# Kernel tuning notes

Measured on AMD Instinct MI355X. Metric: run time of the kernel, lower is better.

The kernel has to match this reference:

```python
import jax, jax.numpy as jnp
import numpy as np

B, C, H, G, NCLS = 32, 256, 128, 128, 2  # graphs, nodes-per-graph==in_channels, hidden, matrix pool, classes
N = B * C                                # total nodes = 8192
E = 131072


def setup_inputs() -> dict:
    key = jax.random.key(0)
    ks = jax.random.split(key, 12)
    gain = 5.0 / 3.0
    xav = gain * np.sqrt(6.0 / (C + C))  # xavier_uniform bound for [C,C]
    return {
        "x": jax.random.normal(ks[0], (N, C), jnp.float32),
        "edge_index": jax.random.randint(ks[1], (2, E), 0, N),
        "graph_id": jax.random.randint(ks[2], (B,), 0, G),
        "batch": jnp.arange(N) // C,
        "pert_W": jax.random.uniform(ks[3], (G, C, C), jnp.float32, -xav, xav),
        "pert_b": jax.random.uniform(ks[4], (G, C, C), jnp.float32, -xav, xav),
        "mask_W": jax.random.uniform(ks[5], (G, C, C), jnp.float32, -xav, xav),
        "gcn_w0": jax.random.normal(ks[6], (C, H), jnp.float32) / np.sqrt(C),
        "gcn_w1": jax.random.normal(ks[7], (H, H), jnp.float32) / np.sqrt(H),
        "gcn_w2": jax.random.normal(ks[8], (H, H), jnp.float32) / np.sqrt(H),
        "mlp_W": jax.random.normal(ks[9], (2 * H, NCLS), jnp.float32) / np.sqrt(2 * H),
        "mlp_b": jnp.zeros((NCLS,), jnp.float32),
    }


def _hard_where(s):
    # MyWhere: 0 if s <= 0.5 else 1
    return jnp.where(s <= 0.5, 0.0, 1.0).astype(s.dtype)


def _predictor(x, adj, batch, gcn_w0, gcn_w1, gcn_w2, mlp_W, mlp_b):
    # GCN encoder: h <- relu(A @ h @ W); readout = concat(mean-pool, max-pool); MLP+sigmoid
    h = x
    for W in (gcn_w0, gcn_w1, gcn_w2):
        h = jax.nn.relu(adj @ (h @ W))
    sums = jax.ops.segment_sum(h, batch, num_segments=B)
    cnt = jax.ops.segment_sum(jnp.ones((h.shape[0], 1), h.dtype), batch, num_segments=B)
    mean = sums / jnp.maximum(cnt, 1.0)
    mx = jax.ops.segment_max(h, batch, num_segments=B)
    pooled = jnp.concatenate([mean, mx], axis=-1)  # [B, 2H]
    return jax.nn.sigmoid(pooled @ mlp_W + mlp_b)


def reference(x, edge_index, graph_id, batch, pert_W, pert_b, mask_W,
              gcn_w0, gcn_w1, gcn_w2, mlp_W, mlp_b):
    # dense adjacency (duplicate edges sum, matching sparse_coo.to_dense)
    adj = jnp.zeros((N, N), jnp.float32).at[edge_index[0], edge_index[1]].add(1.0)
    P = pert_W[graph_id]    # [B, C, C] block-diag blocks
    bias = pert_b[graph_id]  # [B, C, C] block-diag bias blocks
    # block_diag(P) @ adj == per-block GEMM over row stripes
    PA = jnp.einsum('bij,bjn->bin', P, adj.reshape(B, C, N))  # [B, C, N]
    PA = PA.reshape(B, C, B, C).at[jnp.arange(B), :, jnp.arange(B), :].add(bias)
    PA = PA.reshape(N, N)
    pert_adj = _hard_where(jax.nn.sigmoid(PA))
    M = _hard_where(jax.nn.sigmoid(mask_W[graph_id].reshape(N, C)))
    x_masked = M * x
    pred = _predictor(x, adj, batch, gcn_w0, gcn_w1, gcn_w2, mlp_W, mlp_b)
    aug_pred = _predictor(x_masked, pert_adj, batch, gcn_w0, gcn_w1, gcn_w2, mlp_W, mlp_b)
    return (adj, pert_adj, M, pred, aug_pred, x_masked)
```

## Files before the change

### kernel.cpp

```cpp
#include <hip/hip_runtime.h>
#include <hip/hip_bf16.h>

#define NN 8192
#define CC 256
#define BBg 32
#define HH 128
#define EE 131072

typedef __attribute__((ext_vector_type(8))) short short8;
typedef __attribute__((ext_vector_type(4))) float f32x4;
typedef unsigned long long ull;

__device__ __forceinline__ float hard01(float v) {
    if (v >= 1e-6f) return 1.0f;
    if (v <= 0.0f) return 0.0f;
    float ef = (float)exp(-(double)v);
    float s = 1.0f / (1.0f + ef);
    return (s > 0.5f) ? 1.0f : 0.0f;
}

__device__ __forceinline__ unsigned short f2bf(float f) {
    unsigned u = __float_as_uint(f);
    u += 0x7FFFu + ((u >> 16) & 1u);
    return (unsigned short)(u >> 16);
}
__device__ __forceinline__ float bf2f(unsigned short b) {
    return __uint_as_float(((unsigned)b) << 16);
}

__global__ void k_hist_mask(const int* __restrict__ ei, int* __restrict__ rowcnt,
                            int* __restrict__ colcnt, unsigned char* __restrict__ coljs,
                            const float* __restrict__ maskW, const int* __restrict__ gid,
                            const float* __restrict__ x, float* __restrict__ Mo,
                            float* __restrict__ xm) {
    int blk = blockIdx.x, t = threadIdx.x;
    if (blk < 512) {
        int e = blk * 256 + t;
        int r = ei[e], c = ei[EE + e];
        atomicAdd(&rowcnt[r], 1);
        int idx = (r >> 8) * NN + c;
        int slot = atomicAdd(&colcnt[idx], 1);
        if (slot < 16) coljs[(size_t)idx * 16 + slot] = (unsigned char)(r & 255);
    } else {
        int i = (blk - 512) * 256 + t;
        int base = i * 4;
        int r = base >> 8;
        int c = base & 255;
        int g = gid[r >> 8];
        float4 mv = *(const float4*)(maskW + ((size_t)g << 16) + ((size_t)(r & 255) << 8) + c);
        float4 xv = *(const float4*)(x + ((size_t)r << 8) + c);
        float4 m, o;
        m.x = hard01(mv.x); m.y = hard01(mv.y); m.z = hard01(mv.z); m.w = hard01(mv.w);
        o.x = m.x * xv.x; o.y = m.y * xv.y; o.z = m.z * xv.z; o.w = m.w * xv.w;
        *(float4*)(Mo + ((size_t)r << 8) + c) = m;
        *(float4*)(xm + ((size_t)r << 8) + c) = o;
    }
}

__global__ void __launch_bounds__(256) k_scan_pertadj(
        const int* __restrict__ rowcnt, int* __restrict__ rowptr,
        int* __restrict__ rowfill,
        const float* __restrict__ pertW, const float* __restrict__ pertB,
        const int* __restrict__ gid, const int* __restrict__ colcnt,
        const unsigned char* __restrict__ coljs,
        float* __restrict__ padj, unsigned char* __restrict__ padjbits) {
    __shared__ float Pl[32][257];
    __shared__ int sums[256];
    int t = threadIdx.x;
    if (blockIdx.x == 0) {
        int base = t * 32;
        int loc[32];
        int s = 0;
        #pragma unroll
        for (int i = 0; i < 32; ++i) { loc[i] = s; s += rowcnt[base + i]; }
        sums[t] = s;
        __syncthreads();
        if (t == 0) {
            int a = 0;
            for (int i = 0; i < 256; ++i) { int v = sums[i]; sums[i] = a; a += v; }
            rowptr[NN] = a;
        }
        __syncthreads();
        int off = sums[t];
        #pragma unroll
        for (int i = 0; i < 32; ++i) {
            rowptr[base + i] = off + loc[i];
            rowfill[base + i] = off + loc[i];
        }
        return;
    }
    int bid = blockIdx.x - 1;
    int nc = bid & 3, rt = (bid >> 2) & 7, b = bid >> 5;
    int g = gid[b];
    const float* src = pertW + ((size_t)g << 16) + (size_t)rt * 32 * CC;
    #pragma unroll 4
    for (int i = 0; i < 32; ++i) Pl[i][t] = src[i * CC + t];
    __syncthreads();
    int ty = t >> 6, tx = t & 63;
    int ro = ty * 8;
    const float* bsrc = pertB + ((size_t)g << 16) + (size_t)(rt * 32 + ro) * CC;
    for (int it = 0; it < 4; ++it) {
        int n0 = nc * 2048 + it * 512 + tx * 8;
        float s[8][8];
        #pragma unroll
        for (int ii = 0; ii < 8; ++ii)
            #pragma unroll
            for (int cc = 0; cc < 8; ++cc) s[ii][cc] = 0.0f;
        #pragma unroll
        for (int half = 0; half < 2; ++half) {
            int n = n0 + half * 4;
            int cidx = b * NN + n;
            int4 cnt4 = *(const int4*)(colcnt + cidx);
            const uint4* jp = (const uint4*)(coljs + (size_t)cidx * 16);
            #pragma unroll
            for (int cc = 0; cc < 4; ++cc) {
                int cnt = (&cnt4.x)[cc];
                cnt = cnt > 16 ? 16 : cnt;
                if (cnt == 0) continue;
                uint4 jv = jp[cc];
                for (int q = 0; q < cnt; ++q) {
                    unsigned word = (q < 8) ? ((q < 4) ? jv.x : jv.y)
                                            : ((q < 12) ? jv.z : jv.w);
                    int j = (word >> ((q & 3) * 8)) & 255;
                    #pragma unroll
                    for (int ii = 0; ii < 8; ++ii) s[ii][half * 4 + cc] += Pl[ro + ii][j];
                }
            }
        }
        bool diag = ((n0 >> 8) == b);
        #pragma unroll
        for (int ii = 0; ii < 8; ++ii) {
            if (diag) {
                const float* bp = bsrc + (size_t)ii * CC + (n0 & 255);
                #pragma unroll
                for (int cc = 0; cc < 8; ++cc) s[ii][cc] += bp[cc];
            }
            float f[8];
            unsigned byte = 0;
            #pragma unroll
            for (int cc = 0; cc < 8; ++cc) {
                f[cc] = hard01(s[ii][cc]);
                if (f[cc] != 0.f) byte |= (1u << cc);
            }
            size_t ob = (size_t)(b * CC + rt * 32 + ro + ii) * NN + n0;
            float4 f0, f1;
            f0.x = f[0]; f0.y = f[1]; f0.z = f[2]; f0.w = f[3];
            f1.x = f[4]; f1.y = f[5]; f1.z = f[6]; f1.w = f[7];
            *(float4*)(padj + ob) = f0;
            *(float4*)(padj + ob + 4) = f1;
            size_t bb = (size_t)(b * CC + rt * 32 + ro + ii) * (NN / 8)
                        + nc * 256 + it * 64 + tx;
            padjbits[bb] = (unsigned char)byte;
        }
    }
}

__device__ __forceinline__ void gemm_dual_body(
        int mt, int t,
        const float* __restrict__ Ap, const float* __restrict__ Aa,
        const float* __restrict__ W, float* __restrict__ Zp,
        unsigned short* __restrict__ Zthi, unsigned short* __restrict__ Ztlo,
        int K, int relu, int aparts, int apstride,
        float (*Alp)[68], float (*Ala)[68], float (*Wl)[132]) {
    int ty = t >> 3, tx = t & 7;
    float accp[16], acca[16];
    #pragma unroll
    for (int u = 0; u < 16; ++u) { accp[u] = 0.0f; acca[u] = 0.0f; }
    for (int kc = 0; kc < K; kc += 64) {
        int row = t >> 3, q = t & 7;
        {
            const float* ap = Ap + (size_t)(mt * 32 + row) * K + kc + q * 8;
            float4 f0 = *(const float4*)ap;
            float4 f1 = *(const float4*)(ap + 4);
            if (relu) {
                f0.x = fmaxf(f0.x, 0.f); f0.y = fmaxf(f0.y, 0.f);
                f0.z = fmaxf(f0.z, 0.f); f0.w = fmaxf(f0.w, 0.f);
                f1.x = fmaxf(f1.x, 0.f); f1.y = fmaxf(f1.y, 0.f);
                f1.z = fmaxf(f1.z, 0.f); f1.w = fmaxf(f1.w, 0.f);
            }
            *(float4*)&Alp[row][q * 8] = f0;
            *(float4*)&Alp[row][q * 8 + 4] = f1;
        }
        {
            const float* ap = Aa + (size_t)(mt * 32 + row) * K + kc + q * 8;
            float4 f0 = *(const float4*)ap;
            float4 f1 = *(const float4*)(ap + 4);
            for (int p = 1; p < aparts; ++p) {
                float4 g0 = *(const float4*)(ap + (size_t)p * apstride);
                float4 g1 = *(const float4*)(ap + (size_t)p * apstride + 4);
                f0.x += g0.x; f0.y += g0.y; f0.z += g0.z; f0.w += g0.w;
                f1.x += g1.x; f1.y += g1.y; f1.z += g1.z; f1.w += g1.w;
            }
            if (relu) {
                f0.x = fmaxf(f0.x, 0.f); f0.y = fmaxf(f0.y, 0.f);
                f0.z = fmaxf(f0.z, 0.f); f0.w = fmaxf(f0.w, 0.f);
                f1.x = fmaxf(f1.x, 0.f); f1.y = fmaxf(f1.y, 0.f);
                f1.z = fmaxf(f1.z, 0.f); f1.w = fmaxf(f1.w, 0.f);
            }
            *(float4*)&Ala[row][q * 8] = f0;
            *(float4*)&Ala[row][q * 8 + 4] = f1;
        }
        {
            int wrow = t >> 2, wq = t & 3;
            const float* wp = W + (size_t)(kc + wrow) * HH + wq * 32;
            #pragma unroll
            for (int u = 0; u < 32; u += 4)
                *(float4*)&Wl[wrow][wq * 32 + u] = *(const float4*)(wp + u);
        }
        __syncthreads();
        #pragma unroll 2
        for (int kk = 0; kk < 64; ++kk) {
            float a = Alp[ty][kk];
            float b2 = Ala[ty][kk];
            #pragma unroll
            for (int u = 0; u < 16; u += 4) {
                float4 wv = *(const float4*)(&Wl[kk][tx * 16 + u]);
                accp[u + 0] += a * wv.x; accp[u + 1] += a * wv.y;
                accp[u + 2] += a * wv.z; accp[u + 3] += a * wv.w;
                acca[u + 0] += b2 * wv.x; acca[u + 1] += b2 * wv.y;
                acca[u + 2] += b2 * wv.z; acca[u + 3] += b2 * wv.w;
            }
        }
        __syncthreads();
    }
    {
        float* cp = Zp + (size_t)(mt * 32 + ty) * HH + tx * 16;
        #pragma unroll
        for (int u = 0; u < 16; u += 4) {
            float4 f;
            f.x = accp[u]; f.y = accp[u + 1]; f.z = accp[u + 2]; f.w = accp[u + 3];
            *(float4*)(cp + u) = f;
        }
    }
    {
        __syncthreads();
        float* Tl = &Wl[0][0];
        #pragma unroll
        for (int u = 0; u < 16; ++u) Tl[ty * 132 + tx * 16 + u] = acca[u];
        __syncthreads();
        int col = t >> 1, half = t & 1;
        unsigned short hu[16] __attribute__((aligned(16)));
        unsigned short lu[16] __attribute__((aligned(16)));
        #pragma unroll
        for (int rr = 0; rr < 16; ++rr) {
            float v = Tl[(half * 16 + rr) * 132 + col];
            unsigned short hb = f2bf(v);
            hu[rr] = hb;
            lu[rr] = f2bf(v - bf2f(hb));
        }
        size_t ob = (size_t)col * NN + mt * 32 + half * 16;
        *(uint4*)(Zthi + ob)     = *(const uint4*)&hu[0];
        *(uint4*)(Zthi + ob + 8) = *(const uint4*)&hu[8];
        *(uint4*)(Ztlo + ob)     = *(const uint4*)&lu[0];
        *(uint4*)(Ztlo + ob + 8) = *(const uint4*)&lu[8];
    }
}

__global__ void __launch_bounds__(256) k_gemm_fill(
        const float* __restrict__ Ap, const float* __restrict__ Aa,
        const float* __restrict__ W, float* __restrict__ Zp,
        unsigned short* __restrict__ Zthi, unsigned short* __restrict__ Ztlo,
        int K, int relu, int aparts, int apstride,
        const int* __restrict__ ei, int* __restrict__ rowfill,
        int* __restrict__ csrcol) {
    __shared__ float Alp[32][68];
    __shared__ float Ala[32][68];
    __shared__ float Wl[64][132];
    int blk = blockIdx.x, t = threadIdx.x;
    if (blk < 256) {
        gemm_dual_body(blk, t, Ap, Aa, W, Zp, Zthi, Ztlo, K, relu, aparts, apstride,
                       Alp, Ala, Wl);
    } else {
        int e = (blk - 256) * 256 + t;
        int r = ei[e], c = ei[EE + e];
        int pos = atomicAdd(&rowfill[r], 1);
        csrcol[pos] = c;
    }
}

__global__ void __launch_bounds__(256) k_gemm_dual(
        const float* __restrict__ Ap, const float* __restrict__ Aa,
        const float* __restrict__ W, float* __restrict__ Zp,
        unsigned short* __restrict__ Zthi, unsigned short* __restrict__ Ztlo,
        int K, int relu, int aparts, int apstride) {
    __shared__ float Alp[32][68];
    __shared__ float Ala[32][68];
    __shared__ float Wl[64][132];
    gemm_dual_body(blockIdx.x, threadIdx.x, Ap, Aa, W, Zp, Zthi, Ztlo,
                   K, relu, aparts, apstride, Alp, Ala, Wl);
}

__device__ __forceinline__ void mfma_body(
        int blk, int t,
        const unsigned char* __restrict__ padjbits,
        const unsigned short* __restrict__ Zthi,
        const unsigned short* __restrict__ Ztlo,
        float* __restrict__ Sp, unsigned short* BhBase, unsigned short* BlBase) {
    int mt = blk & 63, sk = blk >> 6;
    int w = t >> 6, lane = t & 63;
    int quad = lane >> 4, l15 = lane & 15;
    f32x4 acc[2][8];
    #pragma unroll
    for (int m = 0; m < 2; ++m)
        #pragma unroll
        for (int i = 0; i < 8; ++i) acc[m][i] = (f32x4){0.f, 0.f, 0.f, 0.f};
    int bn = t >> 1, bq = t & 1;
    const unsigned short* zh = Zthi + (size_t)bn * NN + sk * 1024 + bq * 16;
    const unsigned short* zl = Ztlo + (size_t)bn * NN + sk * 1024 + bq * 16;
    int row0 = mt * 128 + w * 32 + l15;
    const unsigned* ab[2];
    #pragma unroll
    for (int m = 0; m < 2; ++m)
        ab[m] = (const unsigned*)(padjbits + (size_t)(row0 + m * 16) * (NN / 8)) + sk * 32;
    int ldsw = bn * 40 + bq * 16;
    int bmb = l15 * 40 + quad * 8;
    uint4 rh0, rh1, rl0, rl1;
    unsigned bits[2], nbits[2];
    rh0 = *(const uint4*)(zh + 0);
    rh1 = *(const uint4*)(zh + 8);
    rl0 = *(const uint4*)(zl + 0);
    rl1 = *(const uint4*)(zl + 8);
    #pragma unroll
    for (int m = 0; m < 2; ++m) bits[m] = ab[m][0];
    *(uint4*)(BhBase + ldsw + 0) = rh0;
    *(uint4*)(BhBase + ldsw + 8) = rh1;
    *(uint4*)(BlBase + ldsw + 0) = rl0;
    *(uint4*)(BlBase + ldsw + 8) = rl1;
    __syncthreads();
    for (int st = 0; st < 32; ++st) {
        int cur = st & 1;
        if (st < 31) {
            int k = (st + 1) * 32;
            rh0 = *(const uint4*)(zh + k);
            rh1 = *(const uint4*)(zh + k + 8);
            rl0 = *(const uint4*)(zl + k);
            rl1 = *(const uint4*)(zl + k + 8);
            #pragma unroll
            for (int m = 0; m < 2; ++m) nbits[m] = ab[m][st + 1];
        }
        short8 a[2];
        #pragma unroll
        for (int m = 0; m < 2; ++m) {
            unsigned byte = (bits[m] >> (quad * 8)) & 0xFFu;
            #pragma unroll
            for (int j = 0; j < 8; ++j)
                a[m][j] = (byte & (1u << j)) ? (short)0x3F80 : (short)0;
        }
        const unsigned short* Bh = BhBase + cur * 5120;
        const unsigned short* Bl = BlBase + cur * 5120;
        #pragma unroll
        for (int nt = 0; nt < 8; ++nt) {
            short8 fh = *(const short8*)(Bh + nt * 16 * 40 + bmb);
            short8 fl = *(const short8*)(Bl + nt * 16 * 40 + bmb);
            #pragma unroll
            for (int m = 0; m < 2; ++m) {
                acc[m][nt] = __builtin_amdgcn_mfma_f32_16x16x32_bf16(a[m], fh, acc[m][nt], 0, 0, 0);
                acc[m][nt] = __builtin_amdgcn_mfma_f32_16x16x32_bf16(a[m], fl, acc[m][nt], 0, 0, 0);
            }
        }
        if (st < 31) {
            unsigned short* BhN = BhBase + (1 - cur) * 5120;
            unsigned short* BlN = BlBase + (1 - cur) * 5120;
            *(uint4*)(BhN + ldsw + 0) = rh0;
            *(uint4*)(BhN + ldsw + 8) = rh1;
            *(uint4*)(BlN + ldsw + 0) = rl0;
            *(uint4*)(BlN + ldsw + 8) = rl1;
            #pragma unroll
            for (int m = 0; m < 2; ++m) bits[m] = nbits[m];
        }
        __syncthreads();
    }
    int dc = l15, dr = quad * 4;
    float* base = Sp + (size_t)sk * NN * HH + (size_t)(mt * 128 + w * 32 + dr) * HH;
    #pragma unroll
    for (int m = 0; m < 2; ++m)
        #pragma unroll
        for (int nt = 0; nt < 8; ++nt)
            #pragma unroll
            for (int r = 0; r < 4; ++r)
                base[(size_t)(m * 16 + r) * HH + nt * 16 + dc] = acc[m][nt][r];
}

__device__ __forceinline__ void adj_body(
        int row, int t, int* cnt,
        const int* __restrict__ rowptr, const int* __restrict__ csrcol,
        float* __restrict__ adj) {
    int4 z = make_int4(0, 0, 0, 0);
    #pragma unroll
    for (int i = 0; i < 8; ++i) *(int4*)&cnt[(i * 256 + t) * 4] = z;
    __syncthreads();
    int start = rowptr[row], end = rowptr[row + 1];
    for (int e = start + t; e < end; e += 256) atomicAdd(&cnt[csrcol[e]], 1);
    __syncthreads();
    float* dst = adj + (size_t)row * NN;
    #pragma unroll
    for (int i = 0; i < 8; ++i) {
        int p = i * 1024 + t * 4;
        float4 f;
        f.x = (float)cnt[p + 0]; f.y = (float)cnt[p + 1];
        f.z = (float)cnt[p + 2]; f.w = (float)cnt[p + 3];
        *(float4*)(dst + p) = f;
    }
}

__device__ __forceinline__ void spmm_body(
        int bp, int t,
        const int* __restrict__ rowptr, const int* __restrict__ csrcol,
        const float* __restrict__ Z, float* __restrict__ S) {
    int row = bp * 2 + (t >> 7);
    int col = t & 127;
    int start = rowptr[row], end = rowptr[row + 1];
    float s0 = 0.f, s1 = 0.f;
    int e = start;
    for (; e + 2 <= end; e += 2) {
        int c0 = csrcol[e], c1 = csrcol[e + 1];
        s0 += Z[(size_t)c0 * HH + col];
        s1 += Z[(size_t)c1 * HH + col];
    }
    if (e < end) s0 += Z[(size_t)csrcol[e] * HH + col];
    S[(size_t)row * HH + col] = s0 + s1;
}

__global__ void __launch_bounds__(256) k_mfma_adj_spmm(
        const unsigned char* __restrict__ padjbits,
        const unsigned short* __restrict__ Zthi,
        const unsigned short* __restrict__ Ztlo,
        float* __restrict__ Sp,
        const int* __restrict__ rowptr, const int* __restrict__ csrcol,
        float* __restrict__ adj,
        const float* __restrict__ Z, float* __restrict__ S) {
    __shared__ __align__(16) char smem[40960];
    int blk = blockIdx.x, t = threadIdx.x;
    if (blk < 512) {
        mfma_body(blk, t, padjbits, Zthi, Ztlo, Sp,
                  (unsigned short*)smem, (unsigned short*)(smem + 20480));
    } else if (blk < 512 + NN / 2) {
        spmm_body(blk - 512, t, rowptr, csrcol, Z, S);
    } else {
        adj_body(blk - (512 + NN / 2), t, (int*)smem, rowptr, csrcol, adj);
    }
}

__global__ void __launch_bounds__(256) k_mfma_spmm2(
        const unsigned char* __restrict__ padjbits,
        const unsigned short* __restrict__ Zthi,
        const unsigned short* __restrict__ Ztlo,
        float* __restrict__ Sp,
        const int* __restrict__ rowptr, const int* __restrict__ csrcol,
        const float* __restrict__ Z, float* __restrict__ S) {
    __shared__ __align__(16) char smem[40960];
    int blk = blockIdx.x, t = threadIdx.x;
    if (blk < 512) {
        mfma_body(blk, t, padjbits, Zthi, Ztlo, Sp,
                  (unsigned short*)smem, (unsigned short*)(smem + 20480));
    } else {
        spmm_body(blk - 512, t, rowptr, csrcol, Z, S);
    }
}

__global__ void __launch_bounds__(256) k_pool2(const float* __restrict__ S,
                                               const float* __restrict__ Sp,
                                               const float* __restrict__ mlpW,
                                               const float* __restrict__ mlpb,
                                               float* __restrict__ pred,
                                               float* __restrict__ augp,
                                               int apstride) {
    __shared__ float ps[256], pm[256], pl[256], r0[256], r1[256];
    int aug = blockIdx.x >> 5, g = blockIdx.x & 31, t = threadIdx.x;
    const float* Sb = aug ? Sp : S;
    int parts = aug ? 8 : 1;
    float* outp = aug ? augp : pred;
    int col = t & 127, half = t >> 7;
    const float* base = Sb + (size_t)(g * CC + half * 128) * HH + col;
    float sum = 0.f, mx = -3.0e38f;
    for (int rr = 0; rr < 128; ++rr) {
        float v = base[(size_t)rr * HH];
        for (int p = 1; p < parts; ++p) v += base[(size_t)p * apstride + (size_t)rr * HH];
        v = fmaxf(v, 0.f);
        sum += v;
        mx = fmaxf(mx, v);
    }
    ps[t] = sum; pm[t] = mx;
    __syncthreads();
    if (half == 0) {
        pl[col] = (ps[col] + ps[col + 128]) * (1.0f / 256.0f);
        pl[col + 128] = fmaxf(pm[col], pm[col + 128]);
    }
    __syncthreads();
    r0[t] = pl[t] * mlpW[t * 2 + 0];
    r1[t] = pl[t] * mlpW[t * 2 + 1];
    __syncthreads();
    for (int sft = 128; sft > 0; sft >>= 1) {
        if (t < sft) { r0[t] += r0[t + sft]; r1[t] += r1[t + sft]; }
        __syncthreads();
    }
    if (t == 0) {
        float l0 = r0[0] + mlpb[0];
        float l1 = r1[0] + mlpb[1];
        outp[g * 2 + 0] = 1.0f / (1.0f + expf(-l0));
        outp[g * 2 + 1] = 1.0f / (1.0f + expf(-l1));
    }
}

extern "C" void kernel_launch(void* const* d_in, const int* in_sizes, int n_in,
                              void* d_out, int out_size, void* d_ws, size_t ws_size,
                              hipStream_t stream) {
    (void)in_sizes; (void)n_in; (void)out_size; (void)ws_size;
    const float* x     = (const float*)d_in[0];
    const int*   ei    = (const int*)d_in[1];
    const int*   gid   = (const int*)d_in[2];
    const float* pertW = (const float*)d_in[4];
    const float* pertB = (const float*)d_in[5];
    const float* maskW = (const float*)d_in[6];
    const float* w0    = (const float*)d_in[7];
    const float* w1    = (const float*)d_in[8];
    const float* w2    = (const float*)d_in[9];
    const float* mlpW  = (const float*)d_in[10];
    const float* mlpb  = (const float*)d_in[11];

    float* out  = (float*)d_out;
    float* adj  = out;
    float* padj = out + (size_t)NN * NN;
    float* Mo   = out + 2 * (size_t)NN * NN;
    float* pred = Mo + (size_t)NN * CC;
    float* augp = pred + (size_t)BBg * 2;
    float* xm   = augp + (size_t)BBg * 2;

    char* ws = (char*)d_ws;
    int*            colcnt   = (int*)ws;
    int*            rowcnt   = (int*)(ws + (1 << 20));
    int*            rowptr   = (int*)(ws + (1 << 20) + (64 << 10));
    int*            rowfill  = (int*)(ws + (1 << 20) + (128 << 10));
    unsigned char*  coljs    = (unsigned char*)(ws + (2 << 20));
    int*            csrcol   = (int*)(ws + (6 << 20));
    float*          Z        = (float*)(ws + (7 << 20));
    float*          S        = (float*)(ws + (11 << 20));
    unsigned short* Zthi     = (unsigned short*)(ws + (15 << 20));
    unsigned short* Ztlo     = (unsigned short*)(ws + (17 << 20));
    float*          Sp       = (float*)(ws + (19 << 20));
    unsigned char*  padjbits = (unsigned char*)(ws + (51 << 20));
    const int PS = NN * HH;

    hipMemsetAsync(colcnt, 0, (1 << 20) + (32 << 10), stream);
    k_hist_mask<<<2560, 256, 0, stream>>>(ei, rowcnt, colcnt, coljs,
                                          maskW, gid, x, Mo, xm);
    k_scan_pertadj<<<1025, 256, 0, stream>>>(rowcnt, rowptr, rowfill,
                                             pertW, pertB, gid, colcnt, coljs,
                                             padj, padjbits);
    k_gemm_fill<<<768, 256, 0, stream>>>(x, xm, w0, Z, Zthi, Ztlo, 256, 0, 1, 0,
                                         ei, rowfill, csrcol);
    k_mfma_adj_spmm<<<512 + NN / 2 + NN, 256, 0, stream>>>(
        padjbits, Zthi, Ztlo, Sp, rowptr, csrcol, adj, Z, S);
    k_gemm_dual<<<256, 256, 0, stream>>>(S, Sp, w1, Z, Zthi, Ztlo, 128, 1, 8, PS);
    k_mfma_spmm2<<<512 + NN / 2, 256, 0, stream>>>(
        padjbits, Zthi, Ztlo, Sp, rowptr, csrcol, Z, S);
    k_gemm_dual<<<256, 256, 0, stream>>>(S, Sp, w2, Z, Zthi, Ztlo, 128, 1, 8, PS);
    k_mfma_spmm2<<<512 + NN / 2, 256, 0, stream>>>(
        padjbits, Zthi, Ztlo, Sp, rowptr, csrcol, Z, S);
    k_pool2<<<64, 256, 0, stream>>>(S, Sp, mlpW, mlpb, pred, augp, PS);
}
```

Before: 1.019 ms.

## Retile dense MFMA aggregation to 256x64 tiles and pack adjacency counts as 16-bit

```diff
diff --git a/kernel.cpp b/kernel.cpp
--- a/kernel.cpp
+++ b/kernel.cpp
@@ -296,109 +296,109 @@
         const unsigned short* __restrict__ Zthi,
         const unsigned short* __restrict__ Ztlo,
         float* __restrict__ Sp, unsigned short* BhBase, unsigned short* BlBase) {
-    int mt = blk & 63, sk = blk >> 6;
+    int mt = blk & 31;
+    int ncol = (blk >> 5) & 1;
+    int sk = blk >> 6;
     int w = t >> 6, lane = t & 63;
     int quad = lane >> 4, l15 = lane & 15;
-    f32x4 acc[2][8];
-    #pragma unroll
-    for (int m = 0; m < 2; ++m)
-        #pragma unroll
-        for (int i = 0; i < 8; ++i) acc[m][i] = (f32x4){0.f, 0.f, 0.f, 0.f};
-    int bn = t >> 1, bq = t & 1;
-    const unsigned short* zh = Zthi + (size_t)bn * NN + sk * 1024 + bq * 16;
-    const unsigned short* zl = Ztlo + (size_t)bn * NN + sk * 1024 + bq * 16;
-    int row0 = mt * 128 + w * 32 + l15;
-    const unsigned* ab[2];
-    #pragma unroll
-    for (int m = 0; m < 2; ++m)
+    f32x4 acc[4][4];
+    #pragma unroll
+    for (int m = 0; m < 4; ++m)
+        #pragma unroll
+        for (int i = 0; i < 4; ++i) acc[m][i] = (f32x4){0.f, 0.f, 0.f, 0.f};
+    int bn = t >> 2, sub = t & 3;
+    int bq = sub & 1, hilo = sub >> 1;
+    const unsigned short* zsrc = (hilo ? Ztlo : Zthi)
+        + (size_t)(ncol * 64 + bn) * NN + sk * 1024 + bq * 16;
+    unsigned short* wb = hilo ? BlBase : BhBase;
+    int row0 = mt * 256 + w * 64 + l15;
+    const unsigned* ab[4];
+    #pragma unroll
+    for (int m = 0; m < 4; ++m)
         ab[m] = (const unsigned*)(padjbits + (size_t)(row0 + m * 16) * (NN / 8)) + sk * 32;
     int ldsw = bn * 40 + bq * 16;
     int bmb = l15 * 40 + quad * 8;
-    uint4 rh0, rh1, rl0, rl1;
-    unsigned bits[2], nbits[2];
-    rh0 = *(const uint4*)(zh + 0);
-    rh1 = *(const uint4*)(zh + 8);
-    rl0 = *(const uint4*)(zl + 0);
-    rl1 = *(const uint4*)(zl + 8);
-    #pragma unroll
-    for (int m = 0; m < 2; ++m) bits[m] = ab[m][0];
-    *(uint4*)(BhBase + ldsw + 0) = rh0;
-    *(uint4*)(BhBase + ldsw + 8) = rh1;
-    *(uint4*)(BlBase + ldsw + 0) = rl0;
-    *(uint4*)(BlBase + ldsw + 8) = rl1;
+    uint4 rv0, rv1;
+    unsigned bits[4], nbits[4];
+    rv0 = *(const uint4*)(zsrc + 0);
+    rv1 = *(const uint4*)(zsrc + 8);
+    #pragma unroll
+    for (int m = 0; m < 4; ++m) bits[m] = ab[m][0];
+    *(uint4*)(wb + ldsw + 0) = rv0;
+    *(uint4*)(wb + ldsw + 8) = rv1;
     __syncthreads();
     for (int st = 0; st < 32; ++st) {
         int cur = st & 1;
         if (st < 31) {
             int k = (st + 1) * 32;
-            rh0 = *(const uint4*)(zh + k);
-            rh1 = *(const uint4*)(zh + k + 8);
-            rl0 = *(const uint4*)(zl + k);
-            rl1 = *(const uint4*)(zl + k + 8);
-            #pragma unroll
-            for (int m = 0; m < 2; ++m) nbits[m] = ab[m][st + 1];
-        }
-        short8 a[2];
-        #pragma unroll
-        for (int m = 0; m < 2; ++m) {
+            rv0 = *(const uint4*)(zsrc + k);
+            rv1 = *(const uint4*)(zsrc + k + 8);
+            #pragma unroll
+            for (int m = 0; m < 4; ++m) nbits[m] = ab[m][st + 1];
+        }
+        short8 a[4];
+        #pragma unroll
+        for (int m = 0; m < 4; ++m) {
             unsigned byte = (bits[m] >> (quad * 8)) & 0xFFu;
             #pragma unroll
             for (int j = 0; j < 8; ++j)
                 a[m][j] = (byte & (1u << j)) ? (short)0x3F80 : (short)0;
         }
-        const unsigned short* Bh = BhBase + cur * 5120;
-        const unsigned short* Bl = BlBase + cur * 5120;
-        #pragma unroll
-        for (int nt = 0; nt < 8; ++nt) {
+        const unsigned short* Bh = BhBase + cur * 2560;
+        const unsigned short* Bl = BlBase + cur * 2560;
+        #pragma unroll
+        for (int nt = 0; nt < 4; ++nt) {
             short8 fh = *(const short8*)(Bh + nt * 16 * 40 + bmb);
             short8 fl = *(const short8*)(Bl + nt * 16 * 40 + bmb);
             #pragma unroll
-            for (int m = 0; m < 2; ++m) {
+            for (int m = 0; m < 4; ++m) {
                 acc[m][nt] = __builtin_amdgcn_mfma_f32_16x16x32_bf16(a[m], fh, acc[m][nt], 0, 0, 0);
                 acc[m][nt] = __builtin_amdgcn_mfma_f32_16x16x32_bf16(a[m], fl, acc[m][nt], 0, 0, 0);
             }
         }
         if (st < 31) {
-            unsigned short* BhN = BhBase + (1 - cur) * 5120;
-            unsigned short* BlN = BlBase + (1 - cur) * 5120;
-            *(uint4*)(BhN + ldsw + 0) = rh0;
-            *(uint4*)(BhN + ldsw + 8) = rh1;
-            *(uint4*)(BlN + ldsw + 0) = rl0;
-            *(uint4*)(BlN + ldsw + 8) = rl1;
-            #pragma unroll
-            for (int m = 0; m < 2; ++m) bits[m] = nbits[m];
+            unsigned short* wn = wb + (1 - cur) * 2560;
+            *(uint4*)(wn + ldsw + 0) = rv0;
+            *(uint4*)(wn + ldsw + 8) = rv1;
+            #pragma unroll
+            for (int m = 0; m < 4; ++m) bits[m] = nbits[m];
         }
         __syncthreads();
     }
     int dc = l15, dr = quad * 4;
-    float* base = Sp + (size_t)sk * NN * HH + (size_t)(mt * 128 + w * 32 + dr) * HH;
-    #pragma unroll
-    for (int m = 0; m < 2; ++m)
-        #pragma unroll
-        for (int nt = 0; nt < 8; ++nt)
+    float* base = Sp + (size_t)sk * NN * HH
+                + (size_t)(mt * 256 + w * 64 + dr) * HH + ncol * 64;
+    #pragma unroll
+    for (int m = 0; m < 4; ++m)
+        #pragma unroll
+        for (int nt = 0; nt < 4; ++nt)
             #pragma unroll
             for (int r = 0; r < 4; ++r)
                 base[(size_t)(m * 16 + r) * HH + nt * 16 + dc] = acc[m][nt][r];
 }
 
 __device__ __forceinline__ void adj_body(
-        int row, int t, int* cnt,
+        int row, int t, unsigned* cnt,
         const int* __restrict__ rowptr, const int* __restrict__ csrcol,
         float* __restrict__ adj) {
-    int4 z = make_int4(0, 0, 0, 0);
-    #pragma unroll
-    for (int i = 0; i < 8; ++i) *(int4*)&cnt[(i * 256 + t) * 4] = z;
+    uint4 z = {0u, 0u, 0u, 0u};
+    #pragma unroll
+    for (int i = 0; i < 4; ++i) *(uint4*)&cnt[(i * 256 + t) * 4] = z;
     __syncthreads();
     int start = rowptr[row], end = rowptr[row + 1];
-    for (int e = start + t; e < end; e += 256) atomicAdd(&cnt[csrcol[e]], 1);
+    for (int e = start + t; e < end; e += 256) {
+        int c = csrcol[e];
+        atomicAdd(&cnt[c >> 1], 1u << ((c & 1) * 16));
+    }
     __syncthreads();
     float* dst = adj + (size_t)row * NN;
     #pragma unroll
     for (int i = 0; i < 8; ++i) {
         int p = i * 1024 + t * 4;
+        unsigned w0 = cnt[p >> 1], w1 = cnt[(p >> 1) + 1];
         float4 f;
-        f.x = (float)cnt[p + 0]; f.y = (float)cnt[p + 1];
-        f.z = (float)cnt[p + 2]; f.w = (float)cnt[p + 3];
+        f.x = (float)(w0 & 0xFFFFu); f.y = (float)(w0 >> 16);
+        f.z = (float)(w1 & 0xFFFFu); f.w = (float)(w1 >> 16);
         *(float4*)(dst + p) = f;
     }
 }
@@ -421,7 +421,10 @@
     S[(size_t)row * HH + col] = s0 + s1;
 }
 
-__global__ void __launch_bounds__(256) k_mfma_adj_spmm(
+#define MFB 1024
+#define SPB (NN / 2)
+
+__global__ void __launch_bounds__(256, 4) k_mfma_adj_spmm(
         const unsigned char* __restrict__ padjbits,
         const unsigned short* __restrict__ Zthi,
         const unsigned short* __restrict__ Ztlo,
@@ -429,32 +432,32 @@
         const int* __restrict__ rowptr, const int* __restrict__ csrcol,
         float* __restrict__ adj,
         const float* __restrict__ Z, float* __restrict__ S) {
-    __shared__ __align__(16) char smem[40960];
+    __shared__ __align__(16) char smem[20480];
     int blk = blockIdx.x, t = threadIdx.x;
-    if (blk < 512) {
+    if (blk < MFB) {
         mfma_body(blk, t, padjbits, Zthi, Ztlo, Sp,
-                  (unsigned short*)smem, (unsigned short*)(smem + 20480));
-    } else if (blk < 512 + NN / 2) {
-        spmm_body(blk - 512, t, rowptr, csrcol, Z, S);
+                  (unsigned short*)smem, (unsigned short*)(smem + 10240));
+    } else if (blk < MFB + SPB) {
+        spmm_body(blk - MFB, t, rowptr, csrcol, Z, S);
     } else {
-        adj_body(blk - (512 + NN / 2), t, (int*)smem, rowptr, csrcol, adj);
-    }
-}
-
-__global__ void __launch_bounds__(256) k_mfma_spmm2(
+        adj_body(blk - (MFB + SPB), t, (unsigned*)smem, rowptr, csrcol, adj);
+    }
+}
+
+__global__ void __launch_bounds__(256, 4) k_mfma_spmm2(
         const unsigned char* __restrict__ padjbits,
         const unsigned short* __restrict__ Zthi,
         const unsigned short* __restrict__ Ztlo,
         float* __restrict__ Sp,
         const int* __restrict__ rowptr, const int* __restrict__ csrcol,
         const float* __restrict__ Z, float* __restrict__ S) {
-    __shared__ __align__(16) char smem[40960];
+    __shared__ __align__(16) char smem[20480];
     int blk = blockIdx.x, t = threadIdx.x;
-    if (blk < 512) {
+    if (blk < MFB) {
         mfma_body(blk, t, padjbits, Zthi, Ztlo, Sp,
-                  (unsigned short*)smem, (unsigned short*)(smem + 20480));
+                  (unsigned short*)smem, (unsigned short*)(smem + 10240));
     } else {
-        spmm_body(blk - 512, t, rowptr, csrcol, Z, S);
+        spmm_body(blk - MFB, t, rowptr, csrcol, Z, S);
     }
 }
 
@@ -549,13 +552,13 @@
                                              padj, padjbits);
     k_gemm_fill<<<768, 256, 0, stream>>>(x, xm, w0, Z, Zthi, Ztlo, 256, 0, 1, 0,
                                          ei, rowfill, csrcol);
-    k_mfma_adj_spmm<<<512 + NN / 2 + NN, 256, 0, stream>>>(
+    k_mfma_adj_spmm<<<MFB + SPB + NN, 256, 0, stream>>>(
         padjbits, Zthi, Ztlo, Sp, rowptr, csrcol, adj, Z, S);
     k_gemm_dual<<<256, 256, 0, stream>>>(S, Sp, w1, Z, Zthi, Ztlo, 128, 1, 8, PS);
-    k_mfma_spmm2<<<512 + NN / 2, 256, 0, stream>>>(
+    k_mfma_spmm2<<<MFB + SPB, 256, 0, stream>>>(
         padjbits, Zthi, Ztlo, Sp, rowptr, csrcol, Z, S);
     k_gemm_dual<<<256, 256, 0, stream>>>(S, Sp, w2, Z, Zthi, Ztlo, 128, 1, 8, PS);
-    k_mfma_spmm2<<<512 + NN / 2, 256, 0, stream>>>(
+    k_mfma_spmm2<<<MFB + SPB, 256, 0, stream>>>(
         padjbits, Zthi, Ztlo, Sp, rowptr, csrcol, Z, S);
     k_pool2<<<64, 256, 0, stream>>>(S, Sp, mlpW, mlpb, pred, augp, PS);
 }
```

Result: slower. 1.112 ms (+9.1%).
